# Optimization experiments

Hardware: AMD Instinct MI355X
Metric: run time of the kernel (lower is better)

Reference implementation:

```python
import jax, jax.numpy as jnp
import numpy as np

B, HQ, S, D = 2, 16, 2048, 64   # batch, query heads, seq len, head dim
DV = 2 * D                      # value head dim (differential attention)
LAMBDA_INIT = 0.8
EPS = 1e-5
NEG = -1.0e9


def setup_inputs() -> dict:
    key = jax.random.key(0)
    ks = jax.random.split(key, 8)
    return {
        "q": jax.random.normal(ks[0], (B, HQ, S, D), dtype=jnp.float32),
        "k": jax.random.normal(ks[1], (B, HQ, S, D), dtype=jnp.float32),
        "v": jax.random.normal(ks[2], (B, HQ // 2, S, DV), dtype=jnp.float32),
        "lambda_q1": jax.random.normal(ks[3], (D,), dtype=jnp.float32) * 0.1,
        "lambda_k1": jax.random.normal(ks[4], (D,), dtype=jnp.float32) * 0.1,
        "lambda_q2": jax.random.normal(ks[5], (D,), dtype=jnp.float32) * 0.1,
        "lambda_k2": jax.random.normal(ks[6], (D,), dtype=jnp.float32) * 0.1,
        "gn_weight": jnp.ones((HQ * D,), dtype=jnp.float32),
        "gn_bias": jnp.zeros((HQ * D,), dtype=jnp.float32),
    }


def ghostmax(scores):
    # softmax with an implicit extra zero logit per row
    m = jnp.maximum(jnp.max(scores, axis=-1, keepdims=True), 0.0)
    e = jnp.exp(scores - m)
    return e / (jnp.sum(e, axis=-1, keepdims=True) + jnp.exp(-m))


def group_norm(x, weight, bias, num_groups, eps):
    # x: [B, C, S]; normalize each group over (C/G, S) like nn.GroupNorm
    b, c, s = x.shape
    xg = x.reshape(b, num_groups, (c // num_groups) * s)
    mean = jnp.mean(xg, axis=-1, keepdims=True)
    var = jnp.var(xg, axis=-1, keepdims=True)
    xn = ((xg - mean) * jax.lax.rsqrt(var + eps)).reshape(b, c, s)
    return xn * weight[None, :, None] + bias[None, :, None]


def reference(q, k, v, lambda_q1, lambda_k1, lambda_q2, lambda_k2, gn_weight, gn_bias):
    scale = 1.0 / np.sqrt(D).astype(np.float32)
    scores = jnp.einsum("bhqd,bhkd->bhqk", q, k) * scale
    causal = jnp.triu(jnp.full((S, S), NEG, dtype=scores.dtype), k=1)
    scores = scores + causal[None, None]
    w = ghostmax(scores)                                   # [B, HQ, S, S]
    w = w.reshape(B, HQ // 2, 2, S, S)
    lam1 = jnp.exp(jnp.sum(lambda_q1 * lambda_k1))
    lam2 = jnp.exp(jnp.sum(lambda_q2 * lambda_k2))
    lam = lam1 - lam2 + LAMBDA_INIT
    w = w[:, :, 0] - lam * w[:, :, 1]                      # [B, HQ/2, S, S]
    out = jnp.einsum("bhqk,bhkd->bhqd", w, v)              # [B, HQ/2, S, DV]
    out = out.reshape(B, HQ * D, S)                        # faithful to torch reshape
    out = group_norm(out, gn_weight, gn_bias, num_groups=HQ, eps=EPS)
    return out * (1.0 - LAMBDA_INIT)
```

## Files before the change

### kernel.cpp

```cpp
#include <hip/hip_runtime.h>
#include <hip/hip_bf16.h>

constexpr int B_ = 2, HQ_ = 16, HP_ = 8, S_ = 2048, D_ = 64, DV_ = 128;
constexpr float LAMB0 = 0.8f;
constexpr float EPSV = 1e-5f;

constexpr int TQ = 64, TK = 32;
constexpr int KSTR = 72;
constexpr int VSTR = 40;

typedef __attribute__((ext_vector_type(8))) short bf16x8;
typedef __attribute__((ext_vector_type(4))) float f32x4;
typedef __attribute__((ext_vector_type(8))) float f32x8;

__device__ __forceinline__ unsigned short f2bf(float x) {
  __hip_bfloat16 h = __float2bfloat16(x);
  unsigned short u;
  __builtin_memcpy(&u, &h, 2);
  return u;
}
__device__ __forceinline__ float bf2f(unsigned short h) {
  return __uint_as_float((unsigned)h << 16);
}
__device__ __forceinline__ unsigned pack2(unsigned short a, unsigned short b) {
  return (unsigned)a | ((unsigned)b << 16);
}
__device__ __forceinline__ void split8v(f32x8 x, bf16x8& hi, bf16x8& lo) {
  union { bf16x8 v; unsigned short s[8]; } H, L;
#pragma unroll
  for (int j = 0; j < 8; ++j) {
    unsigned short h = f2bf(x[j]);
    H.s[j] = h;
    L.s[j] = f2bf(x[j] - bf2f(h));
  }
  hi = H.v;
  lo = L.v;
}

__launch_bounds__(256, 2)
__global__ void diffattn_fwd(const float* __restrict__ qg, const float* __restrict__ kg,
                             const float* __restrict__ vg,
                             const float* __restrict__ lq1, const float* __restrict__ lk1,
                             const float* __restrict__ lq2, const float* __restrict__ lk2,
                             float* __restrict__ Obuf, float* __restrict__ stats) {
  __shared__ short Kl[2][2][TK][KSTR];
  __shared__ short Vt[2][DV_][VSTR];
  __shared__ float redbuf[8];

  const int tid = threadIdx.x;
  const int w = tid >> 6;
  const int l = tid & 63;
  const int g = l >> 4;
  const int li = l & 15;

  const int t = blockIdx.x;
  const int bh = t & 15;
  const int b = bh >> 3;
  const int hp = bh & 7;
  const int u = t >> 4;
  const int qt = (u & 1) ? (31 - (u >> 1)) : (u >> 1);
  const int q0 = qt * TQ;
  const int qw = q0 + w * 16;

  float d1 = 0.f, d2 = 0.f;
  for (int i = 0; i < D_; ++i) { d1 += lq1[i] * lk1[i]; d2 += lq2[i] * lk2[i]; }
  const float lam = __expf(d1) - __expf(d2) + LAMB0;

  bf16x8 qhi[2][2], qlo[2][2];
#pragma unroll
  for (int h = 0; h < 2; ++h)
#pragma unroll
    for (int c = 0; c < 2; ++c) {
      const float* p = qg + (((size_t)b * HQ_ + 2 * hp + h) * S_ + qw + li) * D_ + c * 32 + g * 8;
      f32x8 x = *reinterpret_cast<const f32x8*>(p);
      split8v(x, qhi[h][c], qlo[h][c]);
    }

  float mreg[2] = {0.f, 0.f};
  float lreg[2] = {1.f, 1.f};
  const f32x4 zero4 = {0.f, 0.f, 0.f, 0.f};
  f32x4 Oacc[2][8];
#pragma unroll
  for (int h = 0; h < 2; ++h)
#pragma unroll
    for (int d = 0; d < 8; ++d) Oacc[h][d] = zero4;

  const int khs = tid >> 7;
  const int ktf = tid & 127;
  const float* kb0 = kg + ((size_t)b * HQ_ + 2 * hp + khs) * S_ * D_;
  const int krow0 = ktf >> 3;
  const int kcol8 = (ktf & 7) * 8;
  const int vdv = tid & 127;
  const int vkq0 = tid >> 7;
  const float* vb0 = vg + ((size_t)b * HP_ + hp) * S_ * DV_ + vdv;
  const int vswz = ((vdv >> 3) & 3) << 3;

  const int nkt = (q0 + TQ) / TK;

  for (int kt = 0; kt < nkt; ++kt) {
    const int k0 = kt * TK;
    __syncthreads();

    {
      const float* kb = kb0 + (size_t)k0 * D_;
      f32x8 ka = *reinterpret_cast<const f32x8*>(kb + (size_t)krow0 * D_ + kcol8);
      f32x8 kc = *reinterpret_cast<const f32x8*>(kb + (size_t)(krow0 + 16) * D_ + kcol8);
      const float* vb = vb0 + (size_t)k0 * DV_;
      f32x8 va, vc;
#pragma unroll
      for (int j = 0; j < 8; ++j) va[j] = vb[(size_t)(vkq0 * 8 + j) * DV_];
#pragma unroll
      for (int j = 0; j < 8; ++j) vc[j] = vb[(size_t)(vkq0 * 8 + 16 + j) * DV_];

      bf16x8 hi, lo;
      split8v(ka, hi, lo);
      *reinterpret_cast<bf16x8*>(&Kl[khs][0][krow0][kcol8]) = hi;
      *reinterpret_cast<bf16x8*>(&Kl[khs][1][krow0][kcol8]) = lo;
      split8v(kc, hi, lo);
      *reinterpret_cast<bf16x8*>(&Kl[khs][0][krow0 + 16][kcol8]) = hi;
      *reinterpret_cast<bf16x8*>(&Kl[khs][1][krow0 + 16][kcol8]) = lo;
      split8v(va, hi, lo);
      *reinterpret_cast<bf16x8*>(&Vt[0][vdv][(vkq0 * 8) ^ vswz]) = hi;
      *reinterpret_cast<bf16x8*>(&Vt[1][vdv][(vkq0 * 8) ^ vswz]) = lo;
      split8v(vc, hi, lo);
      *reinterpret_cast<bf16x8*>(&Vt[0][vdv][(vkq0 * 8 + 16) ^ vswz]) = hi;
      *reinterpret_cast<bf16x8*>(&Vt[1][vdv][(vkq0 * 8 + 16) ^ vswz]) = lo;
    }
    __syncthreads();

    if (k0 > qw + 15) continue;
    const bool needmask = (k0 + TK - 1 > qw);
    const int qglob = qw + li;
    bf16x8 AH[2], AL[2];

#pragma unroll
    for (int h = 0; h < 2; ++h) {
      bf16x8 kf[2][2][2];
#pragma unroll
      for (int hl = 0; hl < 2; ++hl)
#pragma unroll
        for (int ms = 0; ms < 2; ++ms)
#pragma unroll
          for (int c = 0; c < 2; ++c)
            kf[hl][ms][c] =
                *reinterpret_cast<const bf16x8*>(&Kl[h][hl][ms * 16 + li][c * 32 + g * 8]);

      f32x4 sT[2] = {zero4, zero4};
      __builtin_amdgcn_s_setprio(1);
#pragma unroll
      for (int ms = 0; ms < 2; ++ms)
#pragma unroll
        for (int c = 0; c < 2; ++c) {
          sT[ms] = __builtin_amdgcn_mfma_f32_16x16x32_bf16(kf[0][ms][c], qhi[h][c], sT[ms], 0, 0, 0);
          sT[ms] = __builtin_amdgcn_mfma_f32_16x16x32_bf16(kf[0][ms][c], qlo[h][c], sT[ms], 0, 0, 0);
          sT[ms] = __builtin_amdgcn_mfma_f32_16x16x32_bf16(kf[1][ms][c], qhi[h][c], sT[ms], 0, 0, 0);
        }
      __builtin_amdgcn_s_setprio(0);

      float sv[2][4];
#pragma unroll
      for (int ms = 0; ms < 2; ++ms)
#pragma unroll
        for (int r = 0; r < 4; ++r) {
          float v = sT[ms][r] * 0.125f;
          if (needmask && (k0 + ms * 16 + g * 4 + r > qglob)) v = -1e30f;
          sv[ms][r] = v;
        }
      float tmax = fmaxf(fmaxf(fmaxf(sv[0][0], sv[0][1]), fmaxf(sv[0][2], sv[0][3])),
                         fmaxf(fmaxf(sv[1][0], sv[1][1]), fmaxf(sv[1][2], sv[1][3])));
      tmax = fmaxf(tmax, __shfl_xor(tmax, 16));
      tmax = fmaxf(tmax, __shfl_xor(tmax, 32));

      if (__any(tmax > mreg[h] + 8.f)) {
        const float mnew = fmaxf(mreg[h], tmax);
        const float fh = __expf(mreg[h] - mnew);
        mreg[h] = mnew;
        lreg[h] *= fh;
        float fr[4];
#pragma unroll
        for (int r = 0; r < 4; ++r) fr[r] = __shfl(fh, 20 * g + r);
#pragma unroll
        for (int d = 0; d < 8; ++d) {
          f32x4 o = Oacc[h][d];
          o[0] *= fr[0]; o[1] *= fr[1]; o[2] *= fr[2]; o[3] *= fr[3];
          Oacc[h][d] = o;
        }
      }

      float p[2][4], psum = 0.f;
#pragma unroll
      for (int ms = 0; ms < 2; ++ms)
#pragma unroll
        for (int r = 0; r < 4; ++r) {
          p[ms][r] = __expf(sv[ms][r] - mreg[h]);
          psum += p[ms][r];
        }
      psum += __shfl_xor(psum, 16);
      psum += __shfl_xor(psum, 32);
      lreg[h] += psum;

      unsigned ph0a = pack2(f2bf(p[0][0]), f2bf(p[0][1]));
      unsigned ph0b = pack2(f2bf(p[0][2]), f2bf(p[0][3]));
      unsigned ph1a = pack2(f2bf(p[1][0]), f2bf(p[1][1]));
      unsigned ph1b = pack2(f2bf(p[1][2]), f2bf(p[1][3]));
      float pl[2][4];
#pragma unroll
      for (int ms = 0; ms < 2; ++ms)
#pragma unroll
        for (int r = 0; r < 4; ++r) pl[ms][r] = p[ms][r] - bf2f(f2bf(p[ms][r]));
      unsigned pl0a = pack2(f2bf(pl[0][0]), f2bf(pl[0][1]));
      unsigned pl0b = pack2(f2bf(pl[0][2]), f2bf(pl[0][3]));
      unsigned pl1a = pack2(f2bf(pl[1][0]), f2bf(pl[1][1]));
      unsigned pl1b = pack2(f2bf(pl[1][2]), f2bf(pl[1][3]));

      const int srcA = 32 * (g & 1) + li;
      const int srcB = srcA + 16;
      const bool hiMs = (g >> 1) != 0;
      union { bf16x8 v; unsigned us[4]; } AHu, ALu;
      {
        unsigned a0 = (unsigned)__shfl((int)ph0a, srcA), b0 = (unsigned)__shfl((int)ph1a, srcA);
        unsigned a1 = (unsigned)__shfl((int)ph0b, srcA), b1 = (unsigned)__shfl((int)ph1b, srcA);
        unsigned a2 = (unsigned)__shfl((int)ph0a, srcB), b2 = (unsigned)__shfl((int)ph1a, srcB);
        unsigned a3 = (unsigned)__shfl((int)ph0b, srcB), b3 = (unsigned)__shfl((int)ph1b, srcB);
        AHu.us[0] = hiMs ? b0 : a0; AHu.us[1] = hiMs ? b1 : a1;
        AHu.us[2] = hiMs ? b2 : a2; AHu.us[3] = hiMs ? b3 : a3;
      }
      {
        unsigned a0 = (unsigned)__shfl((int)pl0a, srcA), b0 = (unsigned)__shfl((int)pl1a, srcA);
        unsigned a1 = (unsigned)__shfl((int)pl0b, srcA), b1 = (unsigned)__shfl((int)pl1b, srcA);
        unsigned a2 = (unsigned)__shfl((int)pl0a, srcB), b2 = (unsigned)__shfl((int)pl1a, srcB);
        unsigned a3 = (unsigned)__shfl((int)pl0b, srcB), b3 = (unsigned)__shfl((int)pl1b, srcB);
        ALu.us[0] = hiMs ? b0 : a0; ALu.us[1] = hiMs ? b1 : a1;
        ALu.us[2] = hiMs ? b2 : a2; ALu.us[3] = hiMs ? b3 : a3;
      }
      AH[h] = AHu.v;
      AL[h] = ALu.v;
    }

    __builtin_amdgcn_s_setprio(1);
#pragma unroll
    for (int dvt = 0; dvt < 8; ++dvt) {
      const int dvr = dvt * 16 + li;
      const int vcol = (g * 8) ^ (((dvr >> 3) & 3) << 3);
      bf16x8 vh = *reinterpret_cast<const bf16x8*>(&Vt[0][dvr][vcol]);
      bf16x8 vl = *reinterpret_cast<const bf16x8*>(&Vt[1][dvr][vcol]);
#pragma unroll
      for (int h = 0; h < 2; ++h) {
        f32x4 acc = Oacc[h][dvt];
        acc = __builtin_amdgcn_mfma_f32_16x16x32_bf16(AH[h], vh, acc, 0, 0, 0);
        acc = __builtin_amdgcn_mfma_f32_16x16x32_bf16(AL[h], vh, acc, 0, 0, 0);
        acc = __builtin_amdgcn_mfma_f32_16x16x32_bf16(AH[h], vl, acc, 0, 0, 0);
        Oacc[h][dvt] = acc;
      }
    }
    __builtin_amdgcn_s_setprio(0);
  }

  float rl0[4], rl1[4];
#pragma unroll
  for (int r = 0; r < 4; ++r) {
    rl0[r] = 1.f / __shfl(lreg[0], 20 * g + r);
    rl1[r] = lam / __shfl(lreg[1], 20 * g + r);
  }
  float* ob = Obuf + ((size_t)(b * HP_ + hp)) * S_ * DV_;
  float lsum = 0.f, lss = 0.f;
#pragma unroll
  for (int dvt = 0; dvt < 8; ++dvt)
#pragma unroll
    for (int r = 0; r < 4; ++r) {
      float vres = Oacc[0][dvt][r] * rl0[r] - Oacc[1][dvt][r] * rl1[r];
      ob[(size_t)(qw + g * 4 + r) * DV_ + dvt * 16 + li] = vres;
      lsum += vres;
      lss += vres * vres;
    }
#pragma unroll
  for (int o = 1; o < 64; o <<= 1) {
    lsum += __shfl_xor(lsum, o);
    lss += __shfl_xor(lss, o);
  }
  if (l == 0) {
    redbuf[w * 2] = lsum;
    redbuf[w * 2 + 1] = lss;
  }
  __syncthreads();
  if (tid == 0) {
    const int region = ((b * HP_ + hp) << 1) | (q0 >= 1024 ? 1 : 0);
    atomicAdd(&stats[2 * region + 0], redbuf[0] + redbuf[2] + redbuf[4] + redbuf[6]);
    atomicAdd(&stats[2 * region + 1], redbuf[1] + redbuf[3] + redbuf[5] + redbuf[7]);
  }
}

__global__ void gn_apply(const float* __restrict__ O, const float* __restrict__ stats,
                         const float* __restrict__ gw, const float* __restrict__ gb,
                         float* __restrict__ out) {
  const size_t f = ((size_t)blockIdx.x * 256 + threadIdx.x) * 4;
  const int g = (int)(f >> 17);
  const int sidx = (int)((f >> 7) & 2047);
  const int hp = (int)((f >> 18) & 7);
  const int c = hp * 128 + (sidx >> 4);
  const float mean = stats[2 * g + 0] * (1.f / 131072.f);
  const float var = stats[2 * g + 1] * (1.f / 131072.f) - mean * mean;
  const float sc = rsqrtf(var + EPSV) * gw[c] * 0.2f;
  const float bi = gb[c] * 0.2f;
  float4 x = *reinterpret_cast<const float4*>(O + f);
  float4 y;
  y.x = (x.x - mean) * sc + bi;
  y.y = (x.y - mean) * sc + bi;
  y.z = (x.z - mean) * sc + bi;
  y.w = (x.w - mean) * sc + bi;
  *reinterpret_cast<float4*>(out + f) = y;
}

extern "C" void kernel_launch(void* const* d_in, const int* in_sizes, int n_in,
                              void* d_out, int out_size, void* d_ws, size_t ws_size,
                              hipStream_t stream) {
  const float* q = (const float*)d_in[0];
  const float* k = (const float*)d_in[1];
  const float* v = (const float*)d_in[2];
  const float* lq1 = (const float*)d_in[3];
  const float* lk1 = (const float*)d_in[4];
  const float* lq2 = (const float*)d_in[5];
  const float* lk2 = (const float*)d_in[6];
  const float* gw = (const float*)d_in[7];
  const float* gb = (const float*)d_in[8];
  float* out = (float*)d_out;

  float* Obuf = (float*)d_ws;
  float* stats = (float*)((char*)d_ws + (size_t)B_ * HP_ * S_ * DV_ * sizeof(float));

  hipMemsetAsync(stats, 0, 64 * sizeof(float), stream);
  diffattn_fwd<<<dim3(512), dim3(256), 0, stream>>>(q, k, v, lq1, lk1, lq2, lk2, Obuf, stats);
  gn_apply<<<dim3(4096), dim3(256), 0, stream>>>(Obuf, stats, gw, gb, out);
}
```

Before: 286.6 us.

## Split the two differential heads across separate waves with LDS combine

Doubles the block to 512 threads so each wave handles one of the two paired heads instead of both, halving per-wave accumulator registers and raising waves per CU. Staging loads are spread over more threads. At the end, the second-head waves write their lambda-scaled output to shared memory (reusing the K/V buffer), and the first-head waves subtract it and compute the group-norm statistics. This adds an extra LDS round-trip and barriers, and the larger block has to fit the register budget set by the new launch bounds.

```diff
diff --git a/kernel.cpp b/kernel.cpp
--- a/kernel.cpp
+++ b/kernel.cpp
@@ -37,18 +37,22 @@
   lo = L.v;
 }
 
-__launch_bounds__(256, 2)
+__launch_bounds__(512, 4)
 __global__ void diffattn_fwd(const float* __restrict__ qg, const float* __restrict__ kg,
                              const float* __restrict__ vg,
                              const float* __restrict__ lq1, const float* __restrict__ lk1,
                              const float* __restrict__ lq2, const float* __restrict__ lk2,
                              float* __restrict__ Obuf, float* __restrict__ stats) {
-  __shared__ short Kl[2][2][TK][KSTR];
-  __shared__ short Vt[2][DV_][VSTR];
+  __shared__ __align__(16) char smem[38912];
+  auto Kl = reinterpret_cast<short(*)[2][TK][KSTR]>(smem);
+  auto Vt = reinterpret_cast<short(*)[DV_][VSTR]>(smem + 18432);
+  float* mbuf = reinterpret_cast<float*>(smem);
   __shared__ float redbuf[8];
 
   const int tid = threadIdx.x;
   const int w = tid >> 6;
+  const int hw = w >> 2;
+  const int qs = w & 3;
   const int l = tid & 63;
   const int g = l >> 4;
   const int li = l & 15;
@@ -60,38 +64,34 @@
   const int u = t >> 4;
   const int qt = (u & 1) ? (31 - (u >> 1)) : (u >> 1);
   const int q0 = qt * TQ;
-  const int qw = q0 + w * 16;
+  const int qw = q0 + qs * 16;
 
   float d1 = 0.f, d2 = 0.f;
   for (int i = 0; i < D_; ++i) { d1 += lq1[i] * lk1[i]; d2 += lq2[i] * lk2[i]; }
   const float lam = __expf(d1) - __expf(d2) + LAMB0;
 
-  bf16x8 qhi[2][2], qlo[2][2];
-#pragma unroll
-  for (int h = 0; h < 2; ++h)
-#pragma unroll
-    for (int c = 0; c < 2; ++c) {
-      const float* p = qg + (((size_t)b * HQ_ + 2 * hp + h) * S_ + qw + li) * D_ + c * 32 + g * 8;
-      f32x8 x = *reinterpret_cast<const f32x8*>(p);
-      split8v(x, qhi[h][c], qlo[h][c]);
-    }
-
-  float mreg[2] = {0.f, 0.f};
-  float lreg[2] = {1.f, 1.f};
+  bf16x8 qhi[2], qlo[2];
+#pragma unroll
+  for (int c = 0; c < 2; ++c) {
+    const float* p = qg + (((size_t)b * HQ_ + 2 * hp + hw) * S_ + qw + li) * D_ + c * 32 + g * 8;
+    f32x8 x = *reinterpret_cast<const f32x8*>(p);
+    split8v(x, qhi[c], qlo[c]);
+  }
+
+  float mreg = 0.f;
+  float lreg = 1.f;
   const f32x4 zero4 = {0.f, 0.f, 0.f, 0.f};
-  f32x4 Oacc[2][8];
-#pragma unroll
-  for (int h = 0; h < 2; ++h)
-#pragma unroll
-    for (int d = 0; d < 8; ++d) Oacc[h][d] = zero4;
-
-  const int khs = tid >> 7;
-  const int ktf = tid & 127;
+  f32x4 Oacc[8];
+#pragma unroll
+  for (int d = 0; d < 8; ++d) Oacc[d] = zero4;
+
+  const int khs = tid >> 8;
+  const int kidx = tid & 255;
+  const int krow = kidx >> 3;
+  const int kcol8 = (kidx & 7) * 8;
   const float* kb0 = kg + ((size_t)b * HQ_ + 2 * hp + khs) * S_ * D_;
-  const int krow0 = ktf >> 3;
-  const int kcol8 = (ktf & 7) * 8;
   const int vdv = tid & 127;
-  const int vkq0 = tid >> 7;
+  const int vk8 = (tid >> 7) * 8;
   const float* vb0 = vg + ((size_t)b * HP_ + hp) * S_ * DV_ + vdv;
   const int vswz = ((vdv >> 3) & 3) << 3;
 
@@ -102,139 +102,126 @@
     __syncthreads();
 
     {
-      const float* kb = kb0 + (size_t)k0 * D_;
-      f32x8 ka = *reinterpret_cast<const f32x8*>(kb + (size_t)krow0 * D_ + kcol8);
-      f32x8 kc = *reinterpret_cast<const f32x8*>(kb + (size_t)(krow0 + 16) * D_ + kcol8);
+      f32x8 kx = *reinterpret_cast<const f32x8*>(kb0 + (size_t)(k0 + krow) * D_ + kcol8);
       const float* vb = vb0 + (size_t)k0 * DV_;
-      f32x8 va, vc;
-#pragma unroll
-      for (int j = 0; j < 8; ++j) va[j] = vb[(size_t)(vkq0 * 8 + j) * DV_];
-#pragma unroll
-      for (int j = 0; j < 8; ++j) vc[j] = vb[(size_t)(vkq0 * 8 + 16 + j) * DV_];
-
+      f32x8 vx;
+#pragma unroll
+      for (int j = 0; j < 8; ++j) vx[j] = vb[(size_t)(vk8 + j) * DV_];
       bf16x8 hi, lo;
-      split8v(ka, hi, lo);
-      *reinterpret_cast<bf16x8*>(&Kl[khs][0][krow0][kcol8]) = hi;
-      *reinterpret_cast<bf16x8*>(&Kl[khs][1][krow0][kcol8]) = lo;
-      split8v(kc, hi, lo);
-      *reinterpret_cast<bf16x8*>(&Kl[khs][0][krow0 + 16][kcol8]) = hi;
-      *reinterpret_cast<bf16x8*>(&Kl[khs][1][krow0 + 16][kcol8]) = lo;
-      split8v(va, hi, lo);
-      *reinterpret_cast<bf16x8*>(&Vt[0][vdv][(vkq0 * 8) ^ vswz]) = hi;
-      *reinterpret_cast<bf16x8*>(&Vt[1][vdv][(vkq0 * 8) ^ vswz]) = lo;
-      split8v(vc, hi, lo);
-      *reinterpret_cast<bf16x8*>(&Vt[0][vdv][(vkq0 * 8 + 16) ^ vswz]) = hi;
-      *reinterpret_cast<bf16x8*>(&Vt[1][vdv][(vkq0 * 8 + 16) ^ vswz]) = lo;
+      split8v(kx, hi, lo);
+      *reinterpret_cast<bf16x8*>(&Kl[khs][0][krow][kcol8]) = hi;
+      *reinterpret_cast<bf16x8*>(&Kl[khs][1][krow][kcol8]) = lo;
+      split8v(vx, hi, lo);
+      *reinterpret_cast<bf16x8*>(&Vt[0][vdv][vk8 ^ vswz]) = hi;
+      *reinterpret_cast<bf16x8*>(&Vt[1][vdv][vk8 ^ vswz]) = lo;
     }
     __syncthreads();
 
     if (k0 > qw + 15) continue;
     const bool needmask = (k0 + TK - 1 > qw);
     const int qglob = qw + li;
-    bf16x8 AH[2], AL[2];
-
-#pragma unroll
-    for (int h = 0; h < 2; ++h) {
-      bf16x8 kf[2][2][2];
-#pragma unroll
-      for (int hl = 0; hl < 2; ++hl)
-#pragma unroll
-        for (int ms = 0; ms < 2; ++ms)
-#pragma unroll
-          for (int c = 0; c < 2; ++c)
-            kf[hl][ms][c] =
-                *reinterpret_cast<const bf16x8*>(&Kl[h][hl][ms * 16 + li][c * 32 + g * 8]);
-
-      f32x4 sT[2] = {zero4, zero4};
-      __builtin_amdgcn_s_setprio(1);
+
+    bf16x8 kf[2][2][2];
+#pragma unroll
+    for (int hl = 0; hl < 2; ++hl)
 #pragma unroll
       for (int ms = 0; ms < 2; ++ms)
 #pragma unroll
-        for (int c = 0; c < 2; ++c) {
-          sT[ms] = __builtin_amdgcn_mfma_f32_16x16x32_bf16(kf[0][ms][c], qhi[h][c], sT[ms], 0, 0, 0);
-          sT[ms] = __builtin_amdgcn_mfma_f32_16x16x32_bf16(kf[0][ms][c], qlo[h][c], sT[ms], 0, 0, 0);
-          sT[ms] = __builtin_amdgcn_mfma_f32_16x16x32_bf16(kf[1][ms][c], qhi[h][c], sT[ms], 0, 0, 0);
-        }
-      __builtin_amdgcn_s_setprio(0);
-
-      float sv[2][4];
-#pragma unroll
-      for (int ms = 0; ms < 2; ++ms)
-#pragma unroll
-        for (int r = 0; r < 4; ++r) {
-          float v = sT[ms][r] * 0.125f;
-          if (needmask && (k0 + ms * 16 + g * 4 + r > qglob)) v = -1e30f;
-          sv[ms][r] = v;
-        }
-      float tmax = fmaxf(fmaxf(fmaxf(sv[0][0], sv[0][1]), fmaxf(sv[0][2], sv[0][3])),
-                         fmaxf(fmaxf(sv[1][0], sv[1][1]), fmaxf(sv[1][2], sv[1][3])));
-      tmax = fmaxf(tmax, __shfl_xor(tmax, 16));
-      tmax = fmaxf(tmax, __shfl_xor(tmax, 32));
-
-      if (__any(tmax > mreg[h] + 8.f)) {
-        const float mnew = fmaxf(mreg[h], tmax);
-        const float fh = __expf(mreg[h] - mnew);
-        mreg[h] = mnew;
-        lreg[h] *= fh;
-        float fr[4];
-#pragma unroll
-        for (int r = 0; r < 4; ++r) fr[r] = __shfl(fh, 20 * g + r);
-#pragma unroll
-        for (int d = 0; d < 8; ++d) {
-          f32x4 o = Oacc[h][d];
-          o[0] *= fr[0]; o[1] *= fr[1]; o[2] *= fr[2]; o[3] *= fr[3];
-          Oacc[h][d] = o;
-        }
-      }
-
-      float p[2][4], psum = 0.f;
-#pragma unroll
-      for (int ms = 0; ms < 2; ++ms)
-#pragma unroll
-        for (int r = 0; r < 4; ++r) {
-          p[ms][r] = __expf(sv[ms][r] - mreg[h]);
-          psum += p[ms][r];
-        }
-      psum += __shfl_xor(psum, 16);
-      psum += __shfl_xor(psum, 32);
-      lreg[h] += psum;
-
-      unsigned ph0a = pack2(f2bf(p[0][0]), f2bf(p[0][1]));
-      unsigned ph0b = pack2(f2bf(p[0][2]), f2bf(p[0][3]));
-      unsigned ph1a = pack2(f2bf(p[1][0]), f2bf(p[1][1]));
-      unsigned ph1b = pack2(f2bf(p[1][2]), f2bf(p[1][3]));
-      float pl[2][4];
-#pragma unroll
-      for (int ms = 0; ms < 2; ++ms)
-#pragma unroll
-        for (int r = 0; r < 4; ++r) pl[ms][r] = p[ms][r] - bf2f(f2bf(p[ms][r]));
-      unsigned pl0a = pack2(f2bf(pl[0][0]), f2bf(pl[0][1]));
-      unsigned pl0b = pack2(f2bf(pl[0][2]), f2bf(pl[0][3]));
-      unsigned pl1a = pack2(f2bf(pl[1][0]), f2bf(pl[1][1]));
-      unsigned pl1b = pack2(f2bf(pl[1][2]), f2bf(pl[1][3]));
-
-      const int srcA = 32 * (g & 1) + li;
-      const int srcB = srcA + 16;
-      const bool hiMs = (g >> 1) != 0;
-      union { bf16x8 v; unsigned us[4]; } AHu, ALu;
-      {
-        unsigned a0 = (unsigned)__shfl((int)ph0a, srcA), b0 = (unsigned)__shfl((int)ph1a, srcA);
-        unsigned a1 = (unsigned)__shfl((int)ph0b, srcA), b1 = (unsigned)__shfl((int)ph1b, srcA);
-        unsigned a2 = (unsigned)__shfl((int)ph0a, srcB), b2 = (unsigned)__shfl((int)ph1a, srcB);
-        unsigned a3 = (unsigned)__shfl((int)ph0b, srcB), b3 = (unsigned)__shfl((int)ph1b, srcB);
-        AHu.us[0] = hiMs ? b0 : a0; AHu.us[1] = hiMs ? b1 : a1;
-        AHu.us[2] = hiMs ? b2 : a2; AHu.us[3] = hiMs ? b3 : a3;
-      }
-      {
-        unsigned a0 = (unsigned)__shfl((int)pl0a, srcA), b0 = (unsigned)__shfl((int)pl1a, srcA);
-        unsigned a1 = (unsigned)__shfl((int)pl0b, srcA), b1 = (unsigned)__shfl((int)pl1b, srcA);
-        unsigned a2 = (unsigned)__shfl((int)pl0a, srcB), b2 = (unsigned)__shfl((int)pl1a, srcB);
-        unsigned a3 = (unsigned)__shfl((int)pl0b, srcB), b3 = (unsigned)__shfl((int)pl1b, srcB);
-        ALu.us[0] = hiMs ? b0 : a0; ALu.us[1] = hiMs ? b1 : a1;
-        ALu.us[2] = hiMs ? b2 : a2; ALu.us[3] = hiMs ? b3 : a3;
-      }
-      AH[h] = AHu.v;
-      AL[h] = ALu.v;
+        for (int c = 0; c < 2; ++c)
+          kf[hl][ms][c] =
+              *reinterpret_cast<const bf16x8*>(&Kl[hw][hl][ms * 16 + li][c * 32 + g * 8]);
+
+    f32x4 sT[2] = {zero4, zero4};
+    __builtin_amdgcn_s_setprio(1);
+#pragma unroll
+    for (int ms = 0; ms < 2; ++ms)
+#pragma unroll
+      for (int c = 0; c < 2; ++c) {
+        sT[ms] = __builtin_amdgcn_mfma_f32_16x16x32_bf16(kf[0][ms][c], qhi[c], sT[ms], 0, 0, 0);
+        sT[ms] = __builtin_amdgcn_mfma_f32_16x16x32_bf16(kf[0][ms][c], qlo[c], sT[ms], 0, 0, 0);
+        sT[ms] = __builtin_amdgcn_mfma_f32_16x16x32_bf16(kf[1][ms][c], qhi[c], sT[ms], 0, 0, 0);
+      }
+    __builtin_amdgcn_s_setprio(0);
+
+    float sv[2][4];
+#pragma unroll
+    for (int ms = 0; ms < 2; ++ms)
+#pragma unroll
+      for (int r = 0; r < 4; ++r) {
+        float v = sT[ms][r] * 0.125f;
+        if (needmask && (k0 + ms * 16 + g * 4 + r > qglob)) v = -1e30f;
+        sv[ms][r] = v;
+      }
+    float tmax = fmaxf(fmaxf(fmaxf(sv[0][0], sv[0][1]), fmaxf(sv[0][2], sv[0][3])),
+                       fmaxf(fmaxf(sv[1][0], sv[1][1]), fmaxf(sv[1][2], sv[1][3])));
+    tmax = fmaxf(tmax, __shfl_xor(tmax, 16));
+    tmax = fmaxf(tmax, __shfl_xor(tmax, 32));
+
+    if (__any(tmax > mreg + 8.f)) {
+      const float mnew = fmaxf(mreg, tmax);
+      const float fh = __expf(mreg - mnew);
+      mreg = mnew;
+      lreg *= fh;
+      float fr[4];
+#pragma unroll
+      for (int r = 0; r < 4; ++r) fr[r] = __shfl(fh, 20 * g + r);
+#pragma unroll
+      for (int d = 0; d < 8; ++d) {
+        f32x4 o = Oacc[d];
+        o[0] *= fr[0]; o[1] *= fr[1]; o[2] *= fr[2]; o[3] *= fr[3];
+        Oacc[d] = o;
+      }
+    }
+
+    float p[2][4], psum = 0.f;
+#pragma unroll
+    for (int ms = 0; ms < 2; ++ms)
+#pragma unroll
+      for (int r = 0; r < 4; ++r) {
+        p[ms][r] = __expf(sv[ms][r] - mreg);
+        psum += p[ms][r];
+      }
+    psum += __shfl_xor(psum, 16);
+    psum += __shfl_xor(psum, 32);
+    lreg += psum;
+
+    unsigned ph0a = pack2(f2bf(p[0][0]), f2bf(p[0][1]));
+    unsigned ph0b = pack2(f2bf(p[0][2]), f2bf(p[0][3]));
+    unsigned ph1a = pack2(f2bf(p[1][0]), f2bf(p[1][1]));
+    unsigned ph1b = pack2(f2bf(p[1][2]), f2bf(p[1][3]));
+    float pl[2][4];
+#pragma unroll
+    for (int ms = 0; ms < 2; ++ms)
+#pragma unroll
+      for (int r = 0; r < 4; ++r) pl[ms][r] = p[ms][r] - bf2f(f2bf(p[ms][r]));
+    unsigned pl0a = pack2(f2bf(pl[0][0]), f2bf(pl[0][1]));
+    unsigned pl0b = pack2(f2bf(pl[0][2]), f2bf(pl[0][3]));
+    unsigned pl1a = pack2(f2bf(pl[1][0]), f2bf(pl[1][1]));
+    unsigned pl1b = pack2(f2bf(pl[1][2]), f2bf(pl[1][3]));
+
+    const int srcA = 32 * (g & 1) + li;
+    const int srcB = srcA + 16;
+    const bool hiMs = (g >> 1) != 0;
+    bf16x8 AH, AL;
+    {
+      union { bf16x8 v; unsigned us[4]; } U;
+      unsigned a0 = (unsigned)__shfl((int)ph0a, srcA), b0 = (unsigned)__shfl((int)ph1a, srcA);
+      unsigned a1 = (unsigned)__shfl((int)ph0b, srcA), b1 = (unsigned)__shfl((int)ph1b, srcA);
+      unsigned a2 = (unsigned)__shfl((int)ph0a, srcB), b2 = (unsigned)__shfl((int)ph1a, srcB);
+      unsigned a3 = (unsigned)__shfl((int)ph0b, srcB), b3 = (unsigned)__shfl((int)ph1b, srcB);
+      U.us[0] = hiMs ? b0 : a0; U.us[1] = hiMs ? b1 : a1;
+      U.us[2] = hiMs ? b2 : a2; U.us[3] = hiMs ? b3 : a3;
+      AH = U.v;
+    }
+    {
+      union { bf16x8 v; unsigned us[4]; } U;
+      unsigned a0 = (unsigned)__shfl((int)pl0a, srcA), b0 = (unsigned)__shfl((int)pl1a, srcA);
+      unsigned a1 = (unsigned)__shfl((int)pl0b, srcA), b1 = (unsigned)__shfl((int)pl1b, srcA);
+      unsigned a2 = (unsigned)__shfl((int)pl0a, srcB), b2 = (unsigned)__shfl((int)pl1a, srcB);
+      unsigned a3 = (unsigned)__shfl((int)pl0b, srcB), b3 = (unsigned)__shfl((int)pl1b, srcB);
+      U.us[0] = hiMs ? b0 : a0; U.us[1] = hiMs ? b1 : a1;
+      U.us[2] = hiMs ? b2 : a2; U.us[3] = hiMs ? b3 : a3;
+      AL = U.v;
     }
 
     __builtin_amdgcn_s_setprio(1);
@@ -244,43 +231,52 @@
       const int vcol = (g * 8) ^ (((dvr >> 3) & 3) << 3);
       bf16x8 vh = *reinterpret_cast<const bf16x8*>(&Vt[0][dvr][vcol]);
       bf16x8 vl = *reinterpret_cast<const bf16x8*>(&Vt[1][dvr][vcol]);
-#pragma unroll
-      for (int h = 0; h < 2; ++h) {
-        f32x4 acc = Oacc[h][dvt];
-        acc = __builtin_amdgcn_mfma_f32_16x16x32_bf16(AH[h], vh, acc, 0, 0, 0);
-        acc = __builtin_amdgcn_mfma_f32_16x16x32_bf16(AL[h], vh, acc, 0, 0, 0);
-        acc = __builtin_amdgcn_mfma_f32_16x16x32_bf16(AH[h], vl, acc, 0, 0, 0);
-        Oacc[h][dvt] = acc;
-      }
+      f32x4 acc = Oacc[dvt];
+      acc = __builtin_amdgcn_mfma_f32_16x16x32_bf16(AH, vh, acc, 0, 0, 0);
+      acc = __builtin_amdgcn_mfma_f32_16x16x32_bf16(AL, vh, acc, 0, 0, 0);
+      acc = __builtin_amdgcn_mfma_f32_16x16x32_bf16(AH, vl, acc, 0, 0, 0);
+      Oacc[dvt] = acc;
     }
     __builtin_amdgcn_s_setprio(0);
   }
 
-  float rl0[4], rl1[4];
-#pragma unroll
-  for (int r = 0; r < 4; ++r) {
-    rl0[r] = 1.f / __shfl(lreg[0], 20 * g + r);
-    rl1[r] = lam / __shfl(lreg[1], 20 * g + r);
-  }
-  float* ob = Obuf + ((size_t)(b * HP_ + hp)) * S_ * DV_;
+  __syncthreads();
+  if (w >= 4) {
+    float rl[4];
+#pragma unroll
+    for (int r = 0; r < 4; ++r) rl[r] = lam / __shfl(lreg, 20 * g + r);
+#pragma unroll
+    for (int dvt = 0; dvt < 8; ++dvt)
+#pragma unroll
+      for (int r = 0; r < 4; ++r)
+        mbuf[((qs * 32 + dvt * 4 + r) * 64) + l] = Oacc[dvt][r] * rl[r];
+  }
+  __syncthreads();
+
   float lsum = 0.f, lss = 0.f;
-#pragma unroll
-  for (int dvt = 0; dvt < 8; ++dvt)
-#pragma unroll
-    for (int r = 0; r < 4; ++r) {
-      float vres = Oacc[0][dvt][r] * rl0[r] - Oacc[1][dvt][r] * rl1[r];
-      ob[(size_t)(qw + g * 4 + r) * DV_ + dvt * 16 + li] = vres;
-      lsum += vres;
-      lss += vres * vres;
-    }
-#pragma unroll
-  for (int o = 1; o < 64; o <<= 1) {
-    lsum += __shfl_xor(lsum, o);
-    lss += __shfl_xor(lss, o);
-  }
-  if (l == 0) {
-    redbuf[w * 2] = lsum;
-    redbuf[w * 2 + 1] = lss;
+  if (w < 4) {
+    float rl[4];
+#pragma unroll
+    for (int r = 0; r < 4; ++r) rl[r] = 1.f / __shfl(lreg, 20 * g + r);
+    float* ob = Obuf + ((size_t)(b * HP_ + hp)) * S_ * DV_;
+#pragma unroll
+    for (int dvt = 0; dvt < 8; ++dvt)
+#pragma unroll
+      for (int r = 0; r < 4; ++r) {
+        float vres = Oacc[dvt][r] * rl[r] - mbuf[((qs * 32 + dvt * 4 + r) * 64) + l];
+        ob[(size_t)(qw + g * 4 + r) * DV_ + dvt * 16 + li] = vres;
+        lsum += vres;
+        lss += vres * vres;
+      }
+#pragma unroll
+    for (int o = 1; o < 64; o <<= 1) {
+      lsum += __shfl_xor(lsum, o);
+      lss += __shfl_xor(lss, o);
+    }
+    if (l == 0) {
+      redbuf[w * 2] = lsum;
+      redbuf[w * 2 + 1] = lss;
+    }
   }
   __syncthreads();
   if (tid == 0) {
@@ -329,6 +325,6 @@
   float* stats = (float*)((char*)d_ws + (size_t)B_ * HP_ * S_ * DV_ * sizeof(float));
 
   hipMemsetAsync(stats, 0, 64 * sizeof(float), stream);
-  diffattn_fwd<<<dim3(512), dim3(256), 0, stream>>>(q, k, v, lq1, lk1, lq2, lk2, Obuf, stats);
+  diffattn_fwd<<<dim3(512), dim3(512), 0, stream>>>(q, k, v, lq1, lk1, lq2, lk2, Obuf, stats);
   gn_apply<<<dim3(4096), dim3(256), 0, stream>>>(Obuf, stats, gw, gb, out);
 }
```

Measured after the change: 275.1 us. 4.0% less time.
